# Kernel optimization log

Hardware: AMD Instinct MI355X
Metric: run time of the kernel (lower is better)

The kernel has to match this reference:

```python
import jax, jax.numpy as jnp
import numpy as np

C = 128
H = 4
D = C // H
EPS = 1e-5


def setup_inputs() -> dict:
    key = jax.random.key(0)
    ks = jax.random.split(key, 9)
    B, S = 1, 256
    std = 1.0 / np.sqrt(C)
    return {
        "z_ij": jax.random.normal(ks[0], (B, S, S, C), dtype=jnp.float32),
        "ln_w": jnp.ones((C,), jnp.float32),
        "ln_b": jnp.zeros((C,), jnp.float32),
        "wq": jax.random.normal(ks[1], (C, C), jnp.float32) * std,
        "wk": jax.random.normal(ks[2], (C, C), jnp.float32) * std,
        "wv": jax.random.normal(ks[3], (C, C), jnp.float32) * std,
        "wb": jax.random.normal(ks[4], (C, H), jnp.float32) * std,
        "wg": jax.random.normal(ks[5], (C, C), jnp.float32) * std,
        "wo": jax.random.normal(ks[6], (C, C), jnp.float32) * std,
    }


def reference(z_ij, ln_w, ln_b, wq, wk, wv, wb, wg, wo):
    B, S = z_ij.shape[0], z_ij.shape[1]
    scale = 1.0 / np.sqrt(D)
    # LayerNorm over channel dim
    mu = jnp.mean(z_ij, axis=-1, keepdims=True)
    var = jnp.var(z_ij, axis=-1, keepdims=True)
    zn = (z_ij - mu) * jax.lax.rsqrt(var + EPS) * ln_w + ln_b
    # projections (weights stored input-major: x @ W)
    q = (zn @ wq).reshape(B, S, S, H, D)
    k = (zn @ wk).reshape(B, S, S, H, D)
    v = (zn @ wv).reshape(B, S, S, H, D)
    b = zn @ wb                      # (B,S,S,H)
    g = jax.nn.sigmoid(zn @ wg).reshape(B, S, S, H, D)
    # scores: q at (i,j) vs k at (j,k) -> (B,i,j,H,k); bias broadcast over k
    scores = jnp.einsum("bijhd,bjkhd->bijhk", q, k) * scale + b[..., None]
    alpha = jax.nn.softmax(scores, axis=-1)
    o = jnp.einsum("bijhk,bjkhd->bijhd", alpha, v)
    o = (g * o).reshape(B, S, S, C)
    return o @ wo
```

## Files before the change

### kernel.cpp

```cpp
#include <hip/hip_runtime.h>


#define NROWS 65536

typedef unsigned short u16;
typedef unsigned int   u32;
typedef __attribute__((ext_vector_type(8))) short short8;
typedef __attribute__((ext_vector_type(4))) float f32x4;
typedef __attribute__((ext_vector_type(4))) u32   u32x4;
typedef __attribute__((ext_vector_type(4))) u16   u16x4;
typedef __attribute__((ext_vector_type(8))) u16   u16x8;

__device__ __forceinline__ u16 f2bf(float x) {
    u32 u = __builtin_bit_cast(u32, x);
    return (u16)((u + 0x7fffu + ((u >> 16) & 1u)) >> 16);
}
__device__ __forceinline__ float bf2f(u16 h) {
    u32 u = (u32)h << 16;
    return __builtin_bit_cast(float, u);
}

__global__ __launch_bounds__(256) void prep_w(const float* __restrict__ wq,
                                              const float* __restrict__ wk,
                                              const float* __restrict__ wv,
                                              const float* __restrict__ wg,
                                              u16* __restrict__ wTh,
                                              u16* __restrict__ wTl)
{
    const int gid = blockIdx.x * 256 + threadIdx.x;
    const int k = gid >> 9, n = gid & 511;
    const float* Wm = (n < 128) ? wq : (n < 256) ? wk : (n < 384) ? wv : wg;
    float f = Wm[k * 128 + (n & 127)];
    if (n < 128) f *= 0.17677669529663687f;
    const u16 h = f2bf(f);
    wTh[n * 128 + k] = h;
    wTl[n * 128 + k] = f2bf(f - bf2f(h));
}

__global__ __launch_bounds__(512) void lnproj_kernel(const float* __restrict__ z,
                                                     const float* __restrict__ lnw,
                                                     const float* __restrict__ lnb,
                                                     const u16* __restrict__ wTh,
                                                     const u16* __restrict__ wTl,
                                                     u16* __restrict__ qt2,
                                                     u16* __restrict__ kt2,
                                                     u16* __restrict__ vth,
                                                     u16* __restrict__ vtl,
                                                     float* __restrict__ gb)
{
    const int row0 = blockIdx.x * 64;
    const int tid  = threadIdx.x;

    __shared__ __align__(16) u16 Ah[8192];
    __shared__ __align__(16) u16 Al[8192];

    {
        const int c4 = (tid & 31) * 4;
        const float4 w4 = *(const float4*)(lnw + c4);
        const float4 b4 = *(const float4*)(lnb + c4);
        #pragma unroll
        for (int it = 0; it < 4; ++it) {
            const int row = it * 16 + (tid >> 5);
            const float4 v = *(const float4*)(z + (size_t)(row0 + row) * 128 + c4);
            float s  = v.x + v.y + v.z + v.w;
            float ss = v.x * v.x + v.y * v.y + v.z * v.z + v.w * v.w;
            #pragma unroll
            for (int off = 16; off > 0; off >>= 1) {
                s  += __shfl_xor(s,  off);
                ss += __shfl_xor(ss, off);
            }
            const float mu  = s * (1.0f / 128.0f);
            const float var = ss * (1.0f / 128.0f) - mu * mu;
            const float rs  = rsqrtf(var + 1e-5f);
            float o[4] = {(v.x - mu) * rs * w4.x + b4.x,
                          (v.y - mu) * rs * w4.y + b4.y,
                          (v.z - mu) * rs * w4.z + b4.z,
                          (v.w - mu) * rs * w4.w + b4.w};
            u16x4 hi, lo;
            #pragma unroll
            for (int c = 0; c < 4; ++c) {
                const u16 hx = f2bf(o[c]);
                hi[c] = hx;
                lo[c] = f2bf(o[c] - bf2f(hx));
            }
            const int slot = c4 >> 3, half = (c4 >> 2) & 1;
            const int phys = slot ^ (row & 15);
            *(u16x4*)&Ah[row * 128 + phys * 8 + half * 4] = hi;
            *(u16x4*)&Al[row * 128 + phys * 8 + half * 4] = lo;
        }
    }
    __syncthreads();

    const int w    = tid >> 6;
    const int lane = tid & 63;
    const int g    = lane >> 4;
    const int qc   = lane & 15;

    f32x4 acc[4][4];
    #pragma unroll
    for (int a = 0; a < 4; ++a)
        #pragma unroll
        for (int b = 0; b < 4; ++b) acc[a][b] = (f32x4){0.f, 0.f, 0.f, 0.f};

    #pragma unroll
    for (int kc = 0; kc < 4; ++kc) {
        short8 bh[4], bl[4];
        #pragma unroll
        for (int mt = 0; mt < 4; ++mt) {
            const int row  = mt * 16 + qc;
            const int phys = (kc * 4 + g) ^ (row & 15);
            bh[mt] = *(const short8*)&Ah[row * 128 + phys * 8];
            bl[mt] = *(const short8*)&Al[row * 128 + phys * 8];
        }
        #pragma unroll
        for (int nt = 0; nt < 4; ++nt) {
            const int n_row = w * 64 + nt * 16 + qc;
            const short8 ah = *(const short8*)(wTh + (size_t)n_row * 128 + kc * 32 + g * 8);
            const short8 al = *(const short8*)(wTl + (size_t)n_row * 128 + kc * 32 + g * 8);
            #pragma unroll
            for (int mt = 0; mt < 4; ++mt) {
                acc[nt][mt] = __builtin_amdgcn_mfma_f32_16x16x32_bf16(ah, bh[mt], acc[nt][mt], 0, 0, 0);
                acc[nt][mt] = __builtin_amdgcn_mfma_f32_16x16x32_bf16(ah, bl[mt], acc[nt][mt], 0, 0, 0);
                acc[nt][mt] = __builtin_amdgcn_mfma_f32_16x16x32_bf16(al, bh[mt], acc[nt][mt], 0, 0, 0);
            }
        }
    }

    #pragma unroll
    for (int nt = 0; nt < 4; ++nt) {
        const int nb  = w * 64 + nt * 16 + g * 4;
        const int mat = nb >> 7;
        const int nn  = nb & 127;
        const int h   = nn >> 5, d0 = nn & 31;
        #pragma unroll
        for (int mt = 0; mt < 4; ++mt) {
            const int m = row0 + mt * 16 + qc;
            const f32x4 a = acc[nt][mt];
            if (mat == 3) {
                float4 sg;
                sg.x = 1.0f / (1.0f + __expf(-a[0]));
                sg.y = 1.0f / (1.0f + __expf(-a[1]));
                sg.z = 1.0f / (1.0f + __expf(-a[2]));
                sg.w = 1.0f / (1.0f + __expf(-a[3]));
                *(float4*)(gb + (size_t)m * 128 + nn) = sg;
            } else if (mat == 2) {
                const int j = m >> 8, kk = m & 255;
                #pragma unroll
                for (int r = 0; r < 4; ++r) {
                    const u16 hx = f2bf(a[r]);
                    const size_t idx = ((size_t)(j * 4 + h) * 32 + d0 + r) * 256 + kk;
                    vth[idx] = hx;
                    vtl[idx] = f2bf(a[r] - bf2f(hx));
                }
            } else {
                u16x4 hi, lo;
                #pragma unroll
                for (int c = 0; c < 4; ++c) {
                    const u16 hx = f2bf(a[c]);
                    hi[c] = hx;
                    lo[c] = f2bf(a[c] - bf2f(hx));
                }
                u16* dst;
                if (mat == 0) {
                    const int i = m >> 8, j = m & 255;
                    dst = qt2 + ((size_t)(j * 4 + h) * 256 + i) * 64 + d0;
                } else {
                    const int j = m >> 8, kk = m & 255;
                    dst = kt2 + ((size_t)(j * 4 + h) * 256 + kk) * 64 + d0;
                }
                *(u16x4*)dst        = hi;
                *(u16x4*)(dst + 32) = lo;
            }
        }
    }
}

__global__ __launch_bounds__(512) void attn_kernel(const u16* __restrict__ qt2,
                                                   const u16* __restrict__ kt2,
                                                   const u16* __restrict__ vth,
                                                   const u16* __restrict__ vtl,
                                                   const float* __restrict__ gb,
                                                   float* __restrict__ go)
{
    const int blk  = blockIdx.x;
    const int jh   = blk >> 1;
    const int tid  = threadIdx.x;
    const int q0   = (blk & 1) * 128 + (tid >> 6) * 16;
    const int lane = tid & 63;
    const int g    = lane >> 4;
    const int qc   = lane & 15;

    __shared__ u16 Ks[16384];
    __shared__ u16 Vs[16384];

    {
        const u16* kg = kt2 + (size_t)jh * 16384;
        #pragma unroll
        for (int it = 0; it < 4; ++it) {
            const int t   = it * 512 + tid;
            const int row = t >> 3, c = t & 7;
            const int dc  = c ^ (row & 7);
            *(u16x8*)&Ks[row * 64 + dc * 8] = *(const u16x8*)(kg + t * 8);
        }
        const u16* vhg = vth + (size_t)jh * 8192;
        const u16* vlg = vtl + (size_t)jh * 8192;
        #pragma unroll
        for (int it = 0; it < 2; ++it) {
            const int t   = it * 512 + tid;
            const int row = t >> 5, c = t & 31;
            const int dc  = (c & 24) | ((c & 7) ^ (row & 7));
            *(u16x8*)&Vs[row * 256 + dc * 8] = *(const u16x8*)(vhg + t * 8);
        }
        #pragma unroll
        for (int it = 0; it < 2; ++it) {
            const int t   = it * 512 + tid;
            const int row = t >> 5, c = t & 31;
            const int dc  = (c & 24) | ((c & 7) ^ (row & 7));
            *(u16x8*)&Vs[8192 + row * 256 + dc * 8] = *(const u16x8*)(vlg + t * 8);
        }
    }

    const u16* qrow = qt2 + ((size_t)jh * 256 + q0 + qc) * 64;
    const short8 bqh = *(const short8*)(qrow + g * 8);
    const short8 bql = *(const short8*)(qrow + 32 + g * 8);

    __syncthreads();

    f32x4 st[16];
    #pragma unroll
    for (int t = 0; t < 16; ++t) st[t] = (f32x4){0.f, 0.f, 0.f, 0.f};

    const int slotH = (g ^ (qc & 7)) * 8;
    #pragma unroll
    for (int kt = 0; kt < 16; ++kt) {
        const int rbase = (kt * 16 + qc) * 64;
        const short8 ah = *(const short8*)&Ks[rbase + slotH];
        const short8 al = *(const short8*)&Ks[rbase + (slotH ^ 32)];
        st[kt] = __builtin_amdgcn_mfma_f32_16x16x32_bf16(ah, bqh, st[kt], 0, 0, 0);
        st[kt] = __builtin_amdgcn_mfma_f32_16x16x32_bf16(ah, bql, st[kt], 0, 0, 0);
        st[kt] = __builtin_amdgcn_mfma_f32_16x16x32_bf16(al, bqh, st[kt], 0, 0, 0);
    }

    float m = -1e30f;
    #pragma unroll
    for (int t = 0; t < 16; ++t)
        #pragma unroll
        for (int r = 0; r < 4; ++r) m = fmaxf(m, st[t][r]);
    m = fmaxf(m, __shfl_xor(m, 16));
    m = fmaxf(m, __shfl_xor(m, 32));

    float l = 0.0f;
    #pragma unroll
    for (int t = 0; t < 16; ++t)
        #pragma unroll
        for (int r = 0; r < 4; ++r) {
            const float p = __expf(st[t][r] - m);
            st[t][r] = p;
            l += p;
        }
    l += __shfl_xor(l, 16);
    l += __shfl_xor(l, 32);
    const float inv = 1.0f / l;
    #pragma unroll
    for (int t = 0; t < 16; ++t)
        #pragma unroll
        for (int r = 0; r < 4; ++r) st[t][r] *= inv;

    f32x4 o0 = (f32x4){0.f, 0.f, 0.f, 0.f};
    f32x4 o1 = (f32x4){0.f, 0.f, 0.f, 0.f};
    const int  slA   = qc + 16 * (2 * (g & 1));
    const int  slB   = slA + 16;
    const bool upper = (g >> 1) != 0;

    #pragma unroll
    for (int kc = 0; kc < 8; ++kc) {
        u32 pkh[2][2];
        #pragma unroll
        for (int tt = 0; tt < 2; ++tt)
            #pragma unroll
            for (int u = 0; u < 2; ++u) {
                const float x = st[2 * kc + tt][2 * u];
                const float y = st[2 * kc + tt][2 * u + 1];
                pkh[tt][u] = (u32)f2bf(x) | ((u32)f2bf(y) << 16);
            }
        u32x4 AH;
        #pragma unroll
        for (int j = 0; j < 4; ++j) {
            const int u  = j & 1;
            const int sl = (j < 2) ? slA : slB;
            const u32 h0 = (u32)__shfl((int)pkh[0][u], sl);
            const u32 h1 = (u32)__shfl((int)pkh[1][u], sl);
            AH[j] = upper ? h1 : h0;
        }
        const short8 pah = __builtin_bit_cast(short8, AH);

        const int vc    = (((kc & 1) * 4 + g) ^ (qc & 7));
        const int vslot = ((kc >> 1) * 8 + vc) * 8;
        const short8 b0h = *(const short8*)&Vs[        qc * 256 + vslot];
        const short8 b0l = *(const short8*)&Vs[8192 +  qc * 256 + vslot];
        const short8 b1h = *(const short8*)&Vs[       (16 + qc) * 256 + vslot];
        const short8 b1l = *(const short8*)&Vs[8192 + (16 + qc) * 256 + vslot];
        o0 = __builtin_amdgcn_mfma_f32_16x16x32_bf16(pah, b0h, o0, 0, 0, 0);
        o0 = __builtin_amdgcn_mfma_f32_16x16x32_bf16(pah, b0l, o0, 0, 0, 0);
        o1 = __builtin_amdgcn_mfma_f32_16x16x32_bf16(pah, b1h, o1, 0, 0, 0);
        o1 = __builtin_amdgcn_mfma_f32_16x16x32_bf16(pah, b1l, o1, 0, 0, 0);
    }

    const int jj = jh >> 2, h = jh & 3;
    #pragma unroll
    for (int r = 0; r < 4; ++r) {
        const int qg = q0 + g * 4 + r;
        const size_t base = ((size_t)qg * 256 + jj) * 128 + h * 32 + qc;
        go[base]      = gb[base]      * o0[r];
        go[base + 16] = gb[base + 16] * o1[r];
    }
}

__global__ __launch_bounds__(256) void out_kernel(const float* __restrict__ A,
                                                  const float* __restrict__ W,
                                                  float* __restrict__ out)
{
    const int by   = blockIdx.x;
    const int row0 = by * 128;

    __shared__ float As[32][132];
    __shared__ float Bs[32][132];

    const int tid = threadIdx.x;
    const int tm  = tid & 15, tn = tid >> 4;
    const int m0  = tm * 4,  n0 = tn * 4;

    float acc[8][8];
    #pragma unroll
    for (int a = 0; a < 8; ++a)
        #pragma unroll
        for (int q = 0; q < 8; ++q) acc[a][q] = 0.0f;

    for (int kc = 0; kc < 128; kc += 32) {
        __syncthreads();
        #pragma unroll
        for (int it = 0; it < 4; ++it) {
            const int id = it * 256 + tid;
            const int m  = id >> 3;
            const int kq = (id & 7) * 4;
            const float4 a4 = *(const float4*)(A + (size_t)(row0 + m) * 128 + kc + kq);
            As[kq + 0][m] = a4.x; As[kq + 1][m] = a4.y;
            As[kq + 2][m] = a4.z; As[kq + 3][m] = a4.w;
        }
        #pragma unroll
        for (int it = 0; it < 4; ++it) {
            const int id = it * 256 + tid;
            const int kk = id >> 5;
            const int c4 = (id & 31) * 4;
            *(float4*)&Bs[kk][c4] = *(const float4*)(W + (size_t)(kc + kk) * 128 + c4);
        }
        __syncthreads();
        #pragma unroll
        for (int k = 0; k < 32; ++k) {
            const float4 a0 = *(const float4*)&As[k][m0];
            const float4 a1 = *(const float4*)&As[k][m0 + 64];
            const float4 b0 = *(const float4*)&Bs[k][n0];
            const float4 b1 = *(const float4*)&Bs[k][n0 + 64];
            const float av[8] = {a0.x, a0.y, a0.z, a0.w, a1.x, a1.y, a1.z, a1.w};
            const float bv[8] = {b0.x, b0.y, b0.z, b0.w, b1.x, b1.y, b1.z, b1.w};
            #pragma unroll
            for (int ii = 0; ii < 8; ++ii)
                #pragma unroll
                for (int jj = 0; jj < 8; ++jj)
                    acc[ii][jj] += av[ii] * bv[jj];
        }
    }

    #pragma unroll
    for (int ii = 0; ii < 8; ++ii) {
        const int mA = (ii < 4) ? (m0 + ii) : (m0 + 60 + ii);
        const int r  = row0 + mA;
        #pragma unroll
        for (int nh = 0; nh < 2; ++nh) {
            const int c0 = n0 + nh * 64;
            float4 vv;
            vv.x = acc[ii][nh * 4 + 0]; vv.y = acc[ii][nh * 4 + 1];
            vv.z = acc[ii][nh * 4 + 2]; vv.w = acc[ii][nh * 4 + 3];
            *(float4*)(out + (size_t)r * 128 + c0) = vv;
        }
    }
}

extern "C" void kernel_launch(void* const* d_in, const int* in_sizes, int n_in,
                              void* d_out, int out_size, void* d_ws, size_t ws_size,
                              hipStream_t stream)
{
    const float* z   = (const float*)d_in[0];
    const float* lnw = (const float*)d_in[1];
    const float* lnb = (const float*)d_in[2];
    const float* wq  = (const float*)d_in[3];
    const float* wk  = (const float*)d_in[4];
    const float* wv  = (const float*)d_in[5];
    const float* wg  = (const float*)d_in[7];
    const float* wo  = (const float*)d_in[8];

    const size_t T = (size_t)NROWS * 128;
    float* go  = (float*)d_ws;
    u16*   wTh = (u16*)d_ws;
    u16*   wTl = wTh + 512 * 128;
    float* gb  = (float*)d_ws + T;
    u16*   qt2 = (u16*)(gb + T);
    u16*   kt2 = qt2 + 2 * T;
    u16*   vth = kt2 + 2 * T;
    u16*   vtl = vth + T;

    prep_w       <<<256,  256, 0, stream>>>(wq, wk, wv, wg, wTh, wTl);
    lnproj_kernel<<<1024, 512, 0, stream>>>(z, lnw, lnb, wTh, wTl,
                                            qt2, kt2, vth, vtl, gb);
    attn_kernel  <<<2048, 512, 0, stream>>>(qt2, kt2, vth, vtl, gb, go);
    out_kernel   <<<512,  256, 0, stream>>>(go, wo, (float*)d_out);
}
```

Before: 156.8 us.

## Move output projection to bf16x3 MFMA with hi/lo split operands

The attention kernel now stores the gated output as a packed bf16 hi/lo pair per element instead of fp32. The output projection is rewritten from a scalar FP32 register-tiled GEMM to MFMA 16x16x32 bf16 using three products (hh, hl, lh) to approximate fp32 accuracy. Wo is transposed and split into bf16 fragments held in registers, and A tiles are staged in swizzled LDS. This targets the FP32 FMA cost of the final GEMM, at the price of extra conversion work and a small precision change.

Measured after the change: 155.5 us. Within noise of the previous version (-0.9%).

```diff
diff --git a/kernel.cpp b/kernel.cpp
--- a/kernel.cpp
+++ b/kernel.cpp
@@ -180,7 +180,7 @@
                                                    const u16* __restrict__ vth,
                                                    const u16* __restrict__ vtl,
                                                    const float* __restrict__ gb,
-                                                   float* __restrict__ go)
+                                                   u32* __restrict__ go2)
 {
     const int blk  = blockIdx.x;
     const int jh   = blk >> 1;
@@ -311,77 +311,135 @@
     for (int r = 0; r < 4; ++r) {
         const int qg = q0 + g * 4 + r;
         const size_t base = ((size_t)qg * 256 + jj) * 128 + h * 32 + qc;
-        go[base]      = gb[base]      * o0[r];
-        go[base + 16] = gb[base + 16] * o1[r];
-    }
-}
-
-__global__ __launch_bounds__(256) void out_kernel(const float* __restrict__ A,
-                                                  const float* __restrict__ W,
+        {
+            const float x = gb[base] * o0[r];
+            const u16 hh = f2bf(x);
+            go2[base] = (u32)hh | ((u32)f2bf(x - bf2f(hh)) << 16);
+        }
+        {
+            const float x = gb[base + 16] * o1[r];
+            const u16 hh = f2bf(x);
+            go2[base + 16] = (u32)hh | ((u32)f2bf(x - bf2f(hh)) << 16);
+        }
+    }
+}
+
+__global__ __launch_bounds__(512) void out_kernel(const u32* __restrict__ go2,
+                                                  const float* __restrict__ wo,
                                                   float* __restrict__ out)
 {
-    const int by   = blockIdx.x;
-    const int row0 = by * 128;
-
-    __shared__ float As[32][132];
-    __shared__ float Bs[32][132];
-
-    const int tid = threadIdx.x;
-    const int tm  = tid & 15, tn = tid >> 4;
-    const int m0  = tm * 4,  n0 = tn * 4;
-
-    float acc[8][8];
-    #pragma unroll
-    for (int a = 0; a < 8; ++a)
-        #pragma unroll
-        for (int q = 0; q < 8; ++q) acc[a][q] = 0.0f;
-
-    for (int kc = 0; kc < 128; kc += 32) {
+    const int row0 = blockIdx.x * 128;
+    const int tid  = threadIdx.x;
+
+    __shared__ __align__(16) u16 BUF[32768];
+
+    const int w    = tid >> 6;
+    const int lane = tid & 63;
+    const int g    = lane >> 4;
+    const int qc   = lane & 15;
+    const int wn   = w & 3;
+    const int wm   = w >> 2;
+
+    short8 wfh[4][2], wfl[4][2];
+    {
+        float* WT = (float*)BUF;
+        #pragma unroll
+        for (int p = 0; p < 8; ++p) {
+            const int idx = p * 512 + tid;
+            const int k = idx >> 5, n4 = (idx & 31) * 4;
+            const float4 v = *(const float4*)(wo + k * 128 + n4);
+            const int slot = k >> 3, ins = k & 7;
+            #pragma unroll
+            for (int c = 0; c < 4; ++c) {
+                const int n = n4 + c;
+                WT[n * 128 + ((slot ^ (n & 15)) * 8) + ins] =
+                    (c == 0) ? v.x : (c == 1) ? v.y : (c == 2) ? v.z : v.w;
+            }
+        }
         __syncthreads();
         #pragma unroll
-        for (int it = 0; it < 4; ++it) {
-            const int id = it * 256 + tid;
-            const int m  = id >> 3;
-            const int kq = (id & 7) * 4;
-            const float4 a4 = *(const float4*)(A + (size_t)(row0 + m) * 128 + kc + kq);
-            As[kq + 0][m] = a4.x; As[kq + 1][m] = a4.y;
-            As[kq + 2][m] = a4.z; As[kq + 3][m] = a4.w;
-        }
-        #pragma unroll
-        for (int it = 0; it < 4; ++it) {
-            const int id = it * 256 + tid;
-            const int kk = id >> 5;
-            const int c4 = (id & 31) * 4;
-            *(float4*)&Bs[kk][c4] = *(const float4*)(W + (size_t)(kc + kk) * 128 + c4);
-        }
+        for (int kc = 0; kc < 4; ++kc)
+            #pragma unroll
+            for (int nt = 0; nt < 2; ++nt) {
+                const int n_row = wn * 32 + nt * 16 + qc;
+                const int phys  = (kc * 4 + g) ^ (n_row & 15);
+                const float4 v0 = *(const float4*)&WT[n_row * 128 + phys * 8];
+                const float4 v1 = *(const float4*)&WT[n_row * 128 + phys * 8 + 4];
+                const float vv[8] = {v0.x, v0.y, v0.z, v0.w, v1.x, v1.y, v1.z, v1.w};
+                short8 sh, sl;
+                #pragma unroll
+                for (int e = 0; e < 8; ++e) {
+                    const u16 hx = f2bf(vv[e]);
+                    sh[e] = (short)hx;
+                    sl[e] = (short)f2bf(vv[e] - bf2f(hx));
+                }
+                wfh[kc][nt] = sh;
+                wfl[kc][nt] = sl;
+            }
         __syncthreads();
-        #pragma unroll
-        for (int k = 0; k < 32; ++k) {
-            const float4 a0 = *(const float4*)&As[k][m0];
-            const float4 a1 = *(const float4*)&As[k][m0 + 64];
-            const float4 b0 = *(const float4*)&Bs[k][n0];
-            const float4 b1 = *(const float4*)&Bs[k][n0 + 64];
-            const float av[8] = {a0.x, a0.y, a0.z, a0.w, a1.x, a1.y, a1.z, a1.w};
-            const float bv[8] = {b0.x, b0.y, b0.z, b0.w, b1.x, b1.y, b1.z, b1.w};
-            #pragma unroll
-            for (int ii = 0; ii < 8; ++ii)
-                #pragma unroll
-                for (int jj = 0; jj < 8; ++jj)
-                    acc[ii][jj] += av[ii] * bv[jj];
-        }
-    }
-
-    #pragma unroll
-    for (int ii = 0; ii < 8; ++ii) {
-        const int mA = (ii < 4) ? (m0 + ii) : (m0 + 60 + ii);
-        const int r  = row0 + mA;
-        #pragma unroll
-        for (int nh = 0; nh < 2; ++nh) {
-            const int c0 = n0 + nh * 64;
-            float4 vv;
-            vv.x = acc[ii][nh * 4 + 0]; vv.y = acc[ii][nh * 4 + 1];
-            vv.z = acc[ii][nh * 4 + 2]; vv.w = acc[ii][nh * 4 + 3];
-            *(float4*)(out + (size_t)r * 128 + c0) = vv;
+    }
+
+    u16* Ah = BUF;
+    u16* Al = BUF + 16384;
+    {
+        #pragma unroll
+        for (int p = 0; p < 4; ++p) {
+            const int t   = p * 512 + tid;
+            const int row = t >> 4, c8 = t & 15;
+            const u32* src = go2 + (size_t)(row0 + row) * 128 + c8 * 8;
+            const u32x4 p0 = *(const u32x4*)src;
+            const u32x4 p1 = *(const u32x4*)(src + 4);
+            u16x4 h0, l0, h1, l1;
+            #pragma unroll
+            for (int c = 0; c < 4; ++c) {
+                h0[c] = (u16)(p0[c] & 0xffffu); l0[c] = (u16)(p0[c] >> 16);
+                h1[c] = (u16)(p1[c] & 0xffffu); l1[c] = (u16)(p1[c] >> 16);
+            }
+            const int phys = c8 ^ (row & 15);
+            *(u16x4*)&Ah[row * 128 + phys * 8]     = h0;
+            *(u16x4*)&Ah[row * 128 + phys * 8 + 4] = h1;
+            *(u16x4*)&Al[row * 128 + phys * 8]     = l0;
+            *(u16x4*)&Al[row * 128 + phys * 8 + 4] = l1;
+        }
+    }
+    __syncthreads();
+
+    f32x4 acc[2][4];
+    #pragma unroll
+    for (int a = 0; a < 2; ++a)
+        #pragma unroll
+        for (int b = 0; b < 4; ++b) acc[a][b] = (f32x4){0.f, 0.f, 0.f, 0.f};
+
+    #pragma unroll
+    for (int kc = 0; kc < 4; ++kc) {
+        short8 bh[4], bl[4];
+        #pragma unroll
+        for (int mt = 0; mt < 4; ++mt) {
+            const int row  = wm * 64 + mt * 16 + qc;
+            const int phys = (kc * 4 + g) ^ (row & 15);
+            bh[mt] = *(const short8*)&Ah[row * 128 + phys * 8];
+            bl[mt] = *(const short8*)&Al[row * 128 + phys * 8];
+        }
+        #pragma unroll
+        for (int nt = 0; nt < 2; ++nt)
+            #pragma unroll
+            for (int mt = 0; mt < 4; ++mt) {
+                acc[nt][mt] = __builtin_amdgcn_mfma_f32_16x16x32_bf16(wfh[kc][nt], bh[mt], acc[nt][mt], 0, 0, 0);
+                acc[nt][mt] = __builtin_amdgcn_mfma_f32_16x16x32_bf16(wfh[kc][nt], bl[mt], acc[nt][mt], 0, 0, 0);
+                acc[nt][mt] = __builtin_amdgcn_mfma_f32_16x16x32_bf16(wfl[kc][nt], bh[mt], acc[nt][mt], 0, 0, 0);
+            }
+    }
+
+    #pragma unroll
+    for (int nt = 0; nt < 2; ++nt) {
+        const int n = wn * 32 + nt * 16 + g * 4;
+        #pragma unroll
+        for (int mt = 0; mt < 4; ++mt) {
+            const int m = row0 + wm * 64 + mt * 16 + qc;
+            float4 v;
+            v.x = acc[nt][mt][0]; v.y = acc[nt][mt][1];
+            v.z = acc[nt][mt][2]; v.w = acc[nt][mt][3];
+            *(float4*)(out + (size_t)m * 128 + n) = v;
         }
     }
 }
@@ -400,7 +458,7 @@
     const float* wo  = (const float*)d_in[8];
 
     const size_t T = (size_t)NROWS * 128;
-    float* go  = (float*)d_ws;
+    u32*   go2 = (u32*)d_ws;
     u16*   wTh = (u16*)d_ws;
     u16*   wTl = wTh + 512 * 128;
     float* gb  = (float*)d_ws + T;
@@ -412,6 +470,6 @@
     prep_w       <<<256,  256, 0, stream>>>(wq, wk, wv, wg, wTh, wTl);
     lnproj_kernel<<<1024, 512, 0, stream>>>(z, lnw, lnb, wTh, wTl,
                                             qt2, kt2, vth, vtl, gb);
-    attn_kernel  <<<2048, 512, 0, stream>>>(qt2, kt2, vth, vtl, gb, go);
-    out_kernel   <<<512,  256, 0, stream>>>(go, wo, (float*)d_out);
-}
+    attn_kernel  <<<2048, 512, 0, stream>>>(qt2, kt2, vth, vtl, gb, go2);
+    out_kernel   <<<512,  512, 0, stream>>>(go2, wo, (float*)d_out);
+}
```
